# Performance work log

Measured on AMD Instinct MI355X. Metric: run time of the kernel, lower is better.

## Reference

```python
import jax, jax.numpy as jnp
import numpy as np

B, S, D, H = 2, 2048, 1024, 16
DK = D // H
NEG = -1.0e9

def setup_inputs() -> dict:
    key = jax.random.key(0)
    ks = jax.random.split(key, 12)
    sc = 1.0 / np.sqrt(D)
    q = jax.random.normal(ks[0], (B, S, D), jnp.float32)
    k = jax.random.normal(ks[1], (B, S, D), jnp.float32)
    v = jax.random.normal(ks[2], (B, S, D), jnp.float32)
    # causal mask: True = masked (matches masked_fill(mask == True, -1e9))
    mask = jnp.broadcast_to(jnp.triu(jnp.ones((S, S), bool), k=1)[None, None], (B, 1, S, S))
    Wq = jax.random.normal(ks[3], (D, D), jnp.float32) * sc
    bq = jnp.zeros((D,), jnp.float32)
    Wk = jax.random.normal(ks[4], (D, D), jnp.float32) * sc
    bk = jnp.zeros((D,), jnp.float32)
    Wv = jax.random.normal(ks[5], (D, D), jnp.float32) * sc
    bv = jnp.zeros((D,), jnp.float32)
    Wo = jax.random.normal(ks[6], (D, D), jnp.float32) * sc
    bo = jnp.zeros((D,), jnp.float32)
    return {"q": q, "k": k, "v": v, "mask": mask,
            "Wq": Wq, "bq": bq, "Wk": Wk, "bk": bk,
            "Wv": Wv, "bv": bv, "Wo": Wo, "bo": bo}

def reference(q, k, v, mask, Wq, bq, Wk, bk, Wv, bv, Wo, bo):
    def split_heads(x):  # [B,S,D] -> [B,H,S,DK]
        return x.reshape(B, S, H, DK).transpose(0, 2, 1, 3)
    qh = split_heads(q @ Wq + bq)
    kh = split_heads(k @ Wk + bk)
    vh = split_heads(v @ Wv + bv)
    scores = jnp.einsum('bhqd,bhkd->bhqk', qh, kh) / np.sqrt(DK)
    scores = jnp.where(mask, NEG, scores)
    p = jax.nn.softmax(scores, axis=-1)
    out = jnp.einsum('bhqk,bhkd->bhqd', p, vh)  # [B,H,S,DK]
    out = out.transpose(0, 2, 1, 3).reshape(B, S, D)
    return out @ Wo + bo
```

## Files before the change

kernel.cpp:

```cpp
#include <hip/hip_runtime.h>

#define BB 2
#define SS 2048
#define DD 1024
#define HH 16
#define DKK 64

typedef __attribute__((ext_vector_type(8))) short short8;
typedef __attribute__((ext_vector_type(4))) float floatx4;

__device__ inline float bf2f(ushort u) {
    union { unsigned int i; float f; } x; x.i = ((unsigned int)u) << 16; return x.f;
}
__device__ inline ushort f2bf(float f) {
    union { float f; unsigned int i; } x; x.f = f;
    unsigned int r = x.i + 0x7fff + ((x.i >> 16) & 1);
    return (ushort)(r >> 16);
}
__device__ inline void async_cp16(const ushort* g, ushort* l) {
    __builtin_amdgcn_global_load_lds(
        (const __attribute__((address_space(1))) unsigned int*)g,
        (__attribute__((address_space(3))) unsigned int*)l, 16, 0, 0);
}
__device__ inline unsigned int cvt_pk_bf16(float lo, float hi) {
    unsigned int r;
    asm("v_cvt_pk_bf16_f32 %0, %1, %2" : "=v"(r) : "v"(lo), "v"(hi));
    return r;
}
__device__ inline void swap32(unsigned int& a, unsigned int& b) {
    asm("v_permlane32_swap_b32 %0, %1" : "+v"(a), "+v"(b));
}
__device__ inline void swap16(unsigned int& a, unsigned int& b) {
    asm("v_permlane16_swap_b32 %0, %1" : "+v"(a), "+v"(b));
}

__global__ __launch_bounds__(256) void cvt_w4(const float* __restrict__ w0,
                                              const float* __restrict__ w1,
                                              const float* __restrict__ w2,
                                              const float* __restrict__ w3,
                                              ushort* __restrict__ o0,
                                              ushort* __restrict__ o1,
                                              ushort* __restrict__ o2,
                                              ushort* __restrict__ o3) {
    __shared__ ushort t[32][33];
    int z = blockIdx.z;
    const float* in = (z == 0) ? w0 : (z == 1) ? w1 : (z == 2) ? w2 : w3;
    ushort* out = (z == 0) ? o0 : (z == 1) ? o1 : (z == 2) ? o2 : o3;
    int bx = blockIdx.x, by = blockIdx.y, tx = threadIdx.x;
    for (int i = threadIdx.y; i < 32; i += 8)
        t[i][tx] = f2bf(in[(size_t)(by * 32 + i) * DD + bx * 32 + tx]);
    __syncthreads();
    for (int i = threadIdx.y; i < 32; i += 8)
        out[(size_t)(bx * 32 + i) * DD + by * 32 + tx] = t[tx][i];
}

__global__ __launch_bounds__(256) void cvt_qkv(const float* __restrict__ q,
                                               const float* __restrict__ k,
                                               const float* __restrict__ v,
                                               ushort* __restrict__ oq,
                                               ushort* __restrict__ ok,
                                               ushort* __restrict__ ov) {
    int z = blockIdx.z;
    const float* in = (z == 0) ? q : (z == 1) ? k : v;
    ushort* out = (z == 0) ? oq : (z == 1) ? ok : ov;
    int i = blockIdx.x * 256 + threadIdx.x;
    float4 f0 = ((const float4*)in)[i * 2];
    float4 f1 = ((const float4*)in)[i * 2 + 1];
    short8 p;
    p[0] = (short)f2bf(f0.x); p[1] = (short)f2bf(f0.y);
    p[2] = (short)f2bf(f0.z); p[3] = (short)f2bf(f0.w);
    p[4] = (short)f2bf(f1.x); p[5] = (short)f2bf(f1.y);
    p[6] = (short)f2bf(f1.z); p[7] = (short)f2bf(f1.w);
    ((short8*)out)[i] = p;
}

__global__ __launch_bounds__(256) void gemm_qkv(const ushort* __restrict__ Xq,
                                                const ushort* __restrict__ Xk,
                                                const ushort* __restrict__ Xv,
                                                const ushort* __restrict__ WtQ,
                                                const ushort* __restrict__ WtK,
                                                const ushort* __restrict__ WtV,
                                                const float* __restrict__ bq,
                                                const float* __restrict__ bk,
                                                const float* __restrict__ bv,
                                                ushort* __restrict__ qh,
                                                ushort* __restrict__ kh,
                                                ushort* __restrict__ vt) {
    constexpr int K = 1024;
    constexpr int NT = 32;
    constexpr int LDT = 136;
    __shared__ ushort smem[128 * LDT];

    int lin = blockIdx.x + ((blockIdx.y + (blockIdx.z << 5)) << 3);
    int wid = (lin & 7) * 96 + (lin >> 3);
    int z = wid >> 8;
    int rem = wid & 255;
    int by = rem >> 3, bx = rem & 7;

    const ushort* A  = (z == 0) ? Xq : (z == 1) ? Xk : Xv;
    const ushort* Bt = (z == 0) ? WtQ : (z == 1) ? WtK : WtV;
    const float* bias = (z == 0) ? bq : (z == 1) ? bk : bv;
    ushort* outp = (z == 0) ? qh : (z == 1) ? kh : vt;

    int tid = threadIdx.x;
    int wave = tid >> 6, lane = tid & 63, quad = lane >> 4, l15 = lane & 15;
    int wm = wave >> 1, wn = wave & 1;
    int rowBase = by * 128, colBase = bx * 128;

    auto stage = [&](int k0, int d) {
        int ab = d * 8192, bb2 = 4096 + d * 8192;
#pragma unroll
        for (int j = 0; j < 2; ++j) {
            int cbase = (j * 4 + wave) * 64;
            int c = cbase + lane;
            int row = c >> 2, sub = (c & 3) * 8;
            async_cp16(&A[(size_t)(rowBase + row) * K + k0 + sub], &smem[ab + cbase * 8]);
            async_cp16(&Bt[(size_t)(colBase + row) * K + k0 + sub], &smem[bb2 + cbase * 8]);
        }
    };

    floatx4 acc[4][4] = {};
    stage(0, 0);
    __syncthreads();
    for (int t = 0; t < NT; ++t) {
        if (t + 1 < NT) stage((t + 1) * 32, (t + 1) & 1);
        int ab = (t & 1) * 8192, bb2 = 4096 + (t & 1) * 8192;
        short8 af[4], bf[4];
#pragma unroll
        for (int mi = 0; mi < 4; ++mi)
            af[mi] = *(const short8*)&smem[ab + (wm * 64 + mi * 16 + l15) * 32 + quad * 8];
#pragma unroll
        for (int ni = 0; ni < 4; ++ni)
            bf[ni] = *(const short8*)&smem[bb2 + (wn * 64 + ni * 16 + l15) * 32 + quad * 8];
#pragma unroll
        for (int mi = 0; mi < 4; ++mi)
#pragma unroll
            for (int ni = 0; ni < 4; ++ni)
                acc[mi][ni] = __builtin_amdgcn_mfma_f32_16x16x32_bf16(
                    af[mi], bf[ni], acc[mi][ni], 0, 0, 0);
        __syncthreads();
    }
    if (z == 2) {
        for (int mi = 0; mi < 4; ++mi)
            for (int ni = 0; ni < 4; ++ni) {
                int c = wn * 64 + ni * 16 + l15;
                float bv = bias[colBase + c];
                for (int i = 0; i < 4; ++i) {
                    int r = wm * 64 + mi * 16 + quad * 4 + i;
                    smem[c * LDT + r] = f2bf(acc[mi][ni][i] + bv);
                }
            }
        __syncthreads();
        int b = rowBase >> 11;
        int sBase = rowBase & 2047;
#pragma unroll
        for (int u = 0; u < 8; ++u) {
            int chunk = u * 256 + tid;
            int c = chunk >> 4;
            int r = (chunk & 15) * 8;
            int col = colBase + c, h = col >> 6, dk = col & 63;
            int4 val = *(const int4*)&smem[c * LDT + r];
            *(int4*)&outp[((size_t)((b * HH + h) * DKK + dk)) * SS + sBase + r] = val;
        }
    } else {
        for (int mi = 0; mi < 4; ++mi)
            for (int ni = 0; ni < 4; ++ni) {
                int c = wn * 64 + ni * 16 + l15;
                float bv = bias[colBase + c];
                for (int i = 0; i < 4; ++i) {
                    int r = wm * 64 + mi * 16 + quad * 4 + i;
                    smem[r * LDT + c] = f2bf(acc[mi][ni][i] + bv);
                }
            }
        __syncthreads();
        int bb = rowBase >> 11;
        int sBase = rowBase & 2047;
#pragma unroll
        for (int u = 0; u < 8; ++u) {
            int chunk = u * 256 + tid;
            int r = chunk >> 4;
            int cc = (chunk & 15) * 8;
            int col = colBase + cc, hh = col >> 6, dk = col & 63;
            int4 val = *(const int4*)&smem[r * LDT + cc];
            *(int4*)&outp[((size_t)((bb * HH + hh) * SS + sBase + r)) * DKK + dk] = val;
        }
    }
}

__global__ __launch_bounds__(256) void gemm_fin(const ushort* __restrict__ A,
                                                const ushort* __restrict__ Bt,
                                                const float* __restrict__ bias,
                                                float* __restrict__ outp) {
    constexpr int K = 1024, N = 1024, NT = 32;
    __shared__ ushort smem[12288];
    int tid = threadIdx.x;
    int wave = tid >> 6, lane = tid & 63, quad = lane >> 4, l15 = lane & 15;
    int wm = wave >> 1, wn = wave & 1;

    int lin = blockIdx.x + (blockIdx.y << 3);
    int wid = (lin & 7) * 64 + (lin >> 3);
    int bx = wid & 7, by = wid >> 3;
    int rowBase = by * 64, colBase = bx * 128;

    auto stage = [&](int k0, int d) {
        int ab = d * 6144, bb2 = 2048 + d * 6144;
#pragma unroll
        for (int j = 0; j < 3; ++j) {
            int c = j * 4 + wave;
            int cbase = (c < 4) ? c * 64 : (c - 4) * 64;
            int cc = cbase + lane;
            int row = cc >> 2, sub = (cc & 3) * 8;
            if (c < 4)
                async_cp16(&A[(size_t)(rowBase + row) * K + k0 + sub], &smem[ab + cbase * 8]);
            else
                async_cp16(&Bt[(size_t)(colBase + row) * K + k0 + sub], &smem[bb2 + cbase * 8]);
        }
    };

    floatx4 acc[2][4] = {};
    stage(0, 0);
    __syncthreads();
    for (int t = 0; t < NT; ++t) {
        if (t + 1 < NT) stage((t + 1) * 32, (t + 1) & 1);
        int ab = (t & 1) * 6144, bb2 = 2048 + (t & 1) * 6144;
        short8 af[2], bf[4];
#pragma unroll
        for (int mi = 0; mi < 2; ++mi)
            af[mi] = *(const short8*)&smem[ab + (wm * 32 + mi * 16 + l15) * 32 + quad * 8];
#pragma unroll
        for (int ni = 0; ni < 4; ++ni)
            bf[ni] = *(const short8*)&smem[bb2 + (wn * 64 + ni * 16 + l15) * 32 + quad * 8];
#pragma unroll
        for (int mi = 0; mi < 2; ++mi)
#pragma unroll
            for (int ni = 0; ni < 4; ++ni)
                acc[mi][ni] = __builtin_amdgcn_mfma_f32_16x16x32_bf16(
                    af[mi], bf[ni], acc[mi][ni], 0, 0, 0);
        __syncthreads();
    }
    for (int mi = 0; mi < 2; ++mi)
        for (int ni = 0; ni < 4; ++ni) {
            int col = colBase + wn * 64 + ni * 16 + l15;
            float bv = bias[col];
            for (int i = 0; i < 4; ++i) {
                int row = rowBase + wm * 32 + mi * 16 + quad * 4 + i;
                outp[(size_t)row * N + col] = acc[mi][ni][i] + bv;
            }
        }
}

__global__ __launch_bounds__(256, 2) void flash_attn5(const ushort* __restrict__ qh,
                                                      const ushort* __restrict__ kh,
                                                      const ushort* __restrict__ vt,
                                                      ushort* __restrict__ attn) {
    constexpr int LD = 72;
    __shared__ ushort Ksm[2][64 * LD];
    __shared__ ushort Vsm[2][64 * LD];
    int tid = threadIdx.x;
    int h = blockIdx.y, b = blockIdx.z;
    int wave = tid >> 6, lane = tid & 63, quad = lane >> 4, l15 = lane & 15;
    const size_t headQK = ((size_t)(b * HH + h)) * SS * DKK;
    const size_t headV  = ((size_t)(b * HH + h)) * DKK * SS;
    int c0 = tid, r0 = c0 >> 3, s0 = (c0 & 7) * 8;
    int c1 = tid + 256, r1 = c1 >> 3, s1 = (c1 & 7) * 8;
    const int qt0 = blockIdx.x;
    const int qt1 = 31 - qt0;

    int qrow0 = qt0 * 64 + wave * 16 + l15;
    int qrow1 = qt1 * 64 + wave * 16 + l15;
    short8 q0a = *(const short8*)&qh[headQK + (size_t)qrow0 * DKK + quad * 8];
    short8 q0b = *(const short8*)&qh[headQK + (size_t)qrow0 * DKK + 32 + quad * 8];
    short8 q1a = *(const short8*)&qh[headQK + (size_t)qrow1 * DKK + quad * 8];
    short8 q1b = *(const short8*)&qh[headQK + (size_t)qrow1 * DKK + 32 + quad * 8];

    floatx4 o0[4] = {}, o1[4] = {};
    float l0 = 0.f, l1 = 0.f;
    int qsel = wave * 16 + l15;

    *(int4*)&Ksm[0][r0 * LD + s0] = *(const int4*)&kh[headQK + (size_t)r0 * DKK + s0];
    *(int4*)&Ksm[0][r1 * LD + s1] = *(const int4*)&kh[headQK + (size_t)r1 * DKK + s1];
    *(int4*)&Vsm[0][r0 * LD + s0] = *(const int4*)&vt[headV + (size_t)r0 * SS + s0];
    *(int4*)&Vsm[0][r1 * LD + s1] = *(const int4*)&vt[headV + (size_t)r1 * SS + s1];
    __syncthreads();

    for (int kt = 0; kt <= qt1; ++kt) {
        int cur = kt & 1;
        bool pre = (kt < qt1);
        bool act0 = (kt <= qt0);
        int4 kA, kB, vA, vB;
        if (pre) {
            const ushort* kp = &kh[headQK + (size_t)((kt + 1) * 64) * DKK];
            const ushort* vp = &vt[headV + (kt + 1) * 64];
            kA = *(const int4*)&kp[(size_t)r0 * DKK + s0];
            kB = *(const int4*)&kp[(size_t)r1 * DKK + s1];
            vA = *(const int4*)&vp[(size_t)r0 * SS + s0];
            vB = *(const int4*)&vp[(size_t)r1 * SS + s1];
        }
        floatx4 sv1[4], sv0[4];
#pragma unroll
        for (int cn = 0; cn < 4; ++cn) {
            short8 kf0 = *(const short8*)&Ksm[cur][(cn * 16 + l15) * LD + quad * 8];
            short8 kf1 = *(const short8*)&Ksm[cur][(cn * 16 + l15) * LD + 32 + quad * 8];
            floatx4 z = {};
            z = __builtin_amdgcn_mfma_f32_16x16x32_bf16(kf0, q1a, z, 0, 0, 0);
            z = __builtin_amdgcn_mfma_f32_16x16x32_bf16(kf1, q1b, z, 0, 0, 0);
            sv1[cn] = z;
            if (act0) {
                floatx4 y = {};
                y = __builtin_amdgcn_mfma_f32_16x16x32_bf16(kf0, q0a, y, 0, 0, 0);
                y = __builtin_amdgcn_mfma_f32_16x16x32_bf16(kf1, q0b, y, 0, 0, 0);
                sv0[cn] = y;
            }
        }
        short8 vf[2][4];
#pragma unroll
        for (int ks = 0; ks < 2; ++ks)
#pragma unroll
            for (int n = 0; n < 4; ++n)
                vf[ks][n] = *(const short8*)&Vsm[cur][(n * 16 + l15) * LD + ks * 32 + quad * 8];

        {
            bool diag = (kt == qt1);
            unsigned int pkd[4][2];
#pragma unroll
            for (int cn = 0; cn < 4; ++cn) {
#pragma unroll
                for (int i = 0; i < 4; ++i) {
                    float p = __expf(sv1[cn][i] * 0.125f);
                    if (diag && (cn * 16 + quad * 4 + i) > qsel) p = 0.f;
                    sv1[cn][i] = p;
                    l1 += p;
                }
                pkd[cn][0] = cvt_pk_bf16(sv1[cn][0], sv1[cn][1]);
                pkd[cn][1] = cvt_pk_bf16(sv1[cn][2], sv1[cn][3]);
            }
#pragma unroll
            for (int ks = 0; ks < 2; ++ks) {
                unsigned int a0 = pkd[ks * 2][0], b0 = pkd[ks * 2 + 1][0];
                swap32(a0, b0); swap16(a0, b0);
                unsigned int a1 = pkd[ks * 2][1], b1 = pkd[ks * 2 + 1][1];
                swap32(a1, b1); swap16(a1, b1);
                union { int4 i4; short8 s8; } u;
                u.i4 = make_int4((int)a0, (int)a1, (int)b0, (int)b1);
#pragma unroll
                for (int n = 0; n < 4; ++n)
                    o1[n] = __builtin_amdgcn_mfma_f32_16x16x32_bf16(
                        vf[ks][n], u.s8, o1[n], 0, 0, 0);
            }
        }
        if (act0) {
            bool diag = (kt == qt0);
            unsigned int pkd[4][2];
#pragma unroll
            for (int cn = 0; cn < 4; ++cn) {
#pragma unroll
                for (int i = 0; i < 4; ++i) {
                    float p = __expf(sv0[cn][i] * 0.125f);
                    if (diag && (cn * 16 + quad * 4 + i) > qsel) p = 0.f;
                    sv0[cn][i] = p;
                    l0 += p;
                }
                pkd[cn][0] = cvt_pk_bf16(sv0[cn][0], sv0[cn][1]);
                pkd[cn][1] = cvt_pk_bf16(sv0[cn][2], sv0[cn][3]);
            }
#pragma unroll
            for (int ks = 0; ks < 2; ++ks) {
                unsigned int a0 = pkd[ks * 2][0], b0 = pkd[ks * 2 + 1][0];
                swap32(a0, b0); swap16(a0, b0);
                unsigned int a1 = pkd[ks * 2][1], b1 = pkd[ks * 2 + 1][1];
                swap32(a1, b1); swap16(a1, b1);
                union { int4 i4; short8 s8; } u;
                u.i4 = make_int4((int)a0, (int)a1, (int)b0, (int)b1);
#pragma unroll
                for (int n = 0; n < 4; ++n)
                    o0[n] = __builtin_amdgcn_mfma_f32_16x16x32_bf16(
                        vf[ks][n], u.s8, o0[n], 0, 0, 0);
            }
        }
        if (pre) {
            int nb = cur ^ 1;
            *(int4*)&Ksm[nb][r0 * LD + s0] = kA;
            *(int4*)&Ksm[nb][r1 * LD + s1] = kB;
            *(int4*)&Vsm[nb][r0 * LD + s0] = vA;
            *(int4*)&Vsm[nb][r1 * LD + s1] = vB;
        }
        __syncthreads();
    }
    l0 += __shfl_xor(l0, 16, 64); l0 += __shfl_xor(l0, 32, 64);
    l1 += __shfl_xor(l1, 16, 64); l1 += __shfl_xor(l1, 32, 64);
    float inv0 = 1.0f / l0, inv1 = 1.0f / l1;
    size_t rowOff0 = ((size_t)(b * SS + qt0 * 64 + wave * 16 + l15)) * DD + h * 64;
    size_t rowOff1 = ((size_t)(b * SS + qt1 * 64 + wave * 16 + l15)) * DD + h * 64;
#pragma unroll
    for (int n = 0; n < 4; ++n) {
        int dof = n * 16 + quad * 4;
        int2 v0, v1;
        v0.x = (int)cvt_pk_bf16(o0[n][0] * inv0, o0[n][1] * inv0);
        v0.y = (int)cvt_pk_bf16(o0[n][2] * inv0, o0[n][3] * inv0);
        v1.x = (int)cvt_pk_bf16(o1[n][0] * inv1, o1[n][1] * inv1);
        v1.y = (int)cvt_pk_bf16(o1[n][2] * inv1, o1[n][3] * inv1);
        *(int2*)&attn[rowOff0 + dof] = v0;
        *(int2*)&attn[rowOff1 + dof] = v1;
    }
}

extern "C" void kernel_launch(void* const* d_in, const int* in_sizes, int n_in,
                              void* d_out, int out_size, void* d_ws, size_t ws_size,
                              hipStream_t stream) {
    const float* q  = (const float*)d_in[0];
    const float* k  = (const float*)d_in[1];
    const float* v  = (const float*)d_in[2];
    const float* Wq = (const float*)d_in[4];
    const float* bq = (const float*)d_in[5];
    const float* Wk = (const float*)d_in[6];
    const float* bk = (const float*)d_in[7];
    const float* Wv = (const float*)d_in[8];
    const float* bv = (const float*)d_in[9];
    const float* Wo = (const float*)d_in[10];
    const float* bo = (const float*)d_in[11];

    ushort* ws   = (ushort*)d_ws;
    ushort* WtQ  = ws;
    ushort* WtK  = WtQ + (1u << 20);
    ushort* WtV  = WtK + (1u << 20);
    ushort* WtO  = WtV + (1u << 20);
    ushort* Xv   = WtO + (1u << 20);
    ushort* qh   = Xv + (4u << 20);
    ushort* kh   = qh + (4u << 20);
    ushort* vt   = kh + (4u << 20);
    ushort* Xq   = (ushort*)d_out;
    ushort* Xk   = Xq + (4u << 20);
    ushort* attn = Xv;

    cvt_w4<<<dim3(32, 32, 4), dim3(32, 8), 0, stream>>>(Wq, Wk, Wv, Wo,
                                                        WtQ, WtK, WtV, WtO);
    cvt_qkv<<<dim3(2048, 1, 3), 256, 0, stream>>>(q, k, v, Xq, Xk, Xv);

    gemm_qkv<<<dim3(8, 32, 3), 256, 0, stream>>>(Xq, Xk, Xv, WtQ, WtK, WtV,
                                                 bq, bk, bv, qh, kh, vt);

    flash_attn5<<<dim3(16, 16, 2), 256, 0, stream>>>(qh, kh, vt, attn);

    gemm_fin<<<dim3(8, 64), 256, 0, stream>>>(attn, WtO, bo, (float*)d_out);
}
```

Baseline: 246.0 us.

## Enlarge QKV GEMM tiles to 256x256 with swizzled LDS and manual waitcnt pipelining

Rewrites the QKV projection GEMM to use 512-thread blocks computing 256x256 output tiles with 8x4 MFMA accumulators per wave. LDS reads use an XOR swizzle, and explicit vmcnt waits with raw barriers replace __syncthreads so the next tile's async loads overlap compute. The epilogue now writes directly to global memory instead of staging through LDS. This raises data reuse per block and reduces sync overhead, but it launches only 192 blocks, which may underfill the GPU, and the direct stores are less coalesced.

```diff
diff --git a/kernel.cpp b/kernel.cpp
--- a/kernel.cpp
+++ b/kernel.cpp
@@ -74,116 +74,140 @@
     ((short8*)out)[i] = p;
 }
 
-__global__ __launch_bounds__(256) void gemm_qkv(const ushort* __restrict__ Xq,
-                                                const ushort* __restrict__ Xk,
-                                                const ushort* __restrict__ Xv,
-                                                const ushort* __restrict__ WtQ,
-                                                const ushort* __restrict__ WtK,
-                                                const ushort* __restrict__ WtV,
-                                                const float* __restrict__ bq,
-                                                const float* __restrict__ bk,
-                                                const float* __restrict__ bv,
-                                                ushort* __restrict__ qh,
-                                                ushort* __restrict__ kh,
-                                                ushort* __restrict__ vt) {
+__global__ __launch_bounds__(512, 2) void gemm_qkv(const ushort* __restrict__ Xq,
+                                                   const ushort* __restrict__ Xk,
+                                                   const ushort* __restrict__ Xv,
+                                                   const ushort* __restrict__ WtQ,
+                                                   const ushort* __restrict__ WtK,
+                                                   const ushort* __restrict__ WtV,
+                                                   const float* __restrict__ bq,
+                                                   const float* __restrict__ bk,
+                                                   const float* __restrict__ bv,
+                                                   ushort* __restrict__ qh,
+                                                   ushort* __restrict__ kh,
+                                                   ushort* __restrict__ vt) {
     constexpr int K = 1024;
-    constexpr int NT = 32;
-    constexpr int LDT = 136;
-    __shared__ ushort smem[128 * LDT];
-
-    int lin = blockIdx.x + ((blockIdx.y + (blockIdx.z << 5)) << 3);
-    int wid = (lin & 7) * 96 + (lin >> 3);
-    int z = wid >> 8;
-    int rem = wid & 255;
-    int by = rem >> 3, bx = rem & 7;
-
-    const ushort* A  = (z == 0) ? Xq : (z == 1) ? Xk : Xv;
-    const ushort* Bt = (z == 0) ? WtQ : (z == 1) ? WtK : WtV;
+    constexpr int NKT = 32;
+    __shared__ ushort smem[32768];
+
+    int lin = blockIdx.x + (blockIdx.y << 2) + (blockIdx.z << 6);
+    int wid = (lin & 7) * 24 + (lin >> 3);
+    int z = wid >> 6;
+    int rem = wid & 63;
+    int byy = rem >> 2, bxx = rem & 3;
+    int rowBase = byy * 256, colBase = bxx * 256;
+
+    const ushort* Ag = (z == 0) ? Xq : (z == 1) ? Xk : Xv;
+    const ushort* Bg = (z == 0) ? WtQ : (z == 1) ? WtK : WtV;
     const float* bias = (z == 0) ? bq : (z == 1) ? bk : bv;
     ushort* outp = (z == 0) ? qh : (z == 1) ? kh : vt;
 
     int tid = threadIdx.x;
     int wave = tid >> 6, lane = tid & 63, quad = lane >> 4, l15 = lane & 15;
-    int wm = wave >> 1, wn = wave & 1;
-    int rowBase = by * 128, colBase = bx * 128;
-
-    auto stage = [&](int k0, int d) {
-        int ab = d * 8192, bb2 = 4096 + d * 8192;
-#pragma unroll
-        for (int j = 0; j < 2; ++j) {
-            int cbase = (j * 4 + wave) * 64;
-            int c = cbase + lane;
-            int row = c >> 2, sub = (c & 3) * 8;
-            async_cp16(&A[(size_t)(rowBase + row) * K + k0 + sub], &smem[ab + cbase * 8]);
-            async_cp16(&Bt[(size_t)(colBase + row) * K + k0 + sub], &smem[bb2 + cbase * 8]);
-        }
+    int wm = wave >> 2, wn = wave & 3;
+
+    size_t srcA[2], srcB[2];
+    int dstU[2];
+#pragma unroll
+    for (int r = 0; r < 2; ++r) {
+        int lb = r * 8192 + wave * 1024 + lane * 16;
+        int sl = lb ^ (((lb >> 9) & 1) << 5);
+        int srow = sl >> 6;
+        int scol = (sl & 63) >> 1;
+        srcA[r] = (size_t)(rowBase + srow) * K + scol;
+        srcB[r] = (size_t)(colBase + srow) * K + scol;
+        dstU[r] = r * 4096 + wave * 512;
+    }
+    int aOff[2][4], bOff[4];
+#pragma unroll
+    for (int mh = 0; mh < 2; ++mh)
+#pragma unroll
+        for (int mi = 0; mi < 4; ++mi) {
+            int row = wm * 128 + mh * 64 + mi * 16 + l15;
+            aOff[mh][mi] = row * 32 + ((quad * 8) ^ (((row >> 3) & 1) << 4));
+        }
+#pragma unroll
+    for (int ni = 0; ni < 4; ++ni) {
+        int row = wn * 64 + ni * 16 + l15;
+        bOff[ni] = 8192 + row * 32 + ((quad * 8) ^ (((row >> 3) & 1) << 4));
+    }
+
+    auto stageTile = [&](int u) {
+        int slot = (u & 1) << 14;
+        const ushort* As = Ag + u * 32;
+        const ushort* Bs = Bg + u * 32;
+        async_cp16(As + srcA[0], &smem[slot + dstU[0]]);
+        async_cp16(As + srcA[1], &smem[slot + dstU[1]]);
+        async_cp16(Bs + srcB[0], &smem[slot + 8192 + dstU[0]]);
+        async_cp16(Bs + srcB[1], &smem[slot + 8192 + dstU[1]]);
     };
 
-    floatx4 acc[4][4] = {};
-    stage(0, 0);
-    __syncthreads();
-    for (int t = 0; t < NT; ++t) {
-        if (t + 1 < NT) stage((t + 1) * 32, (t + 1) & 1);
-        int ab = (t & 1) * 8192, bb2 = 4096 + (t & 1) * 8192;
-        short8 af[4], bf[4];
-#pragma unroll
-        for (int mi = 0; mi < 4; ++mi)
-            af[mi] = *(const short8*)&smem[ab + (wm * 64 + mi * 16 + l15) * 32 + quad * 8];
+    floatx4 acc[8][4] = {};
+    stageTile(0);
+    for (int t = 0; t < NKT; ++t) {
+        if (t < NKT - 1) {
+            stageTile(t + 1);
+            asm volatile("s_waitcnt vmcnt(4)" ::: "memory");
+        } else {
+            asm volatile("s_waitcnt vmcnt(0)" ::: "memory");
+        }
+        __builtin_amdgcn_s_barrier();
+        __builtin_amdgcn_sched_barrier(0);
+        int slot = (t & 1) << 14;
+        short8 bfr[4];
 #pragma unroll
         for (int ni = 0; ni < 4; ++ni)
-            bf[ni] = *(const short8*)&smem[bb2 + (wn * 64 + ni * 16 + l15) * 32 + quad * 8];
-#pragma unroll
-        for (int mi = 0; mi < 4; ++mi)
-#pragma unroll
-            for (int ni = 0; ni < 4; ++ni)
-                acc[mi][ni] = __builtin_amdgcn_mfma_f32_16x16x32_bf16(
-                    af[mi], bf[ni], acc[mi][ni], 0, 0, 0);
-        __syncthreads();
-    }
+            bfr[ni] = *(const short8*)&smem[slot + bOff[ni]];
+#pragma unroll
+        for (int mh = 0; mh < 2; ++mh) {
+            short8 af[4];
+#pragma unroll
+            for (int mi = 0; mi < 4; ++mi)
+                af[mi] = *(const short8*)&smem[slot + aOff[mh][mi]];
+#pragma unroll
+            for (int mi = 0; mi < 4; ++mi)
+#pragma unroll
+                for (int ni = 0; ni < 4; ++ni)
+                    acc[mh * 4 + mi][ni] = __builtin_amdgcn_mfma_f32_16x16x32_bf16(
+                        af[mi], bfr[ni], acc[mh * 4 + mi][ni], 0, 0, 0);
+        }
+        __builtin_amdgcn_sched_barrier(0);
+        __builtin_amdgcn_s_barrier();
+    }
+
+    float bvv[4];
+#pragma unroll
+    for (int ni = 0; ni < 4; ++ni)
+        bvv[ni] = bias[colBase + wn * 64 + ni * 16 + l15];
     if (z == 2) {
-        for (int mi = 0; mi < 4; ++mi)
+#pragma unroll
+        for (int mi = 0; mi < 8; ++mi)
+#pragma unroll
             for (int ni = 0; ni < 4; ++ni) {
-                int c = wn * 64 + ni * 16 + l15;
-                float bv = bias[colBase + c];
+                int col = colBase + wn * 64 + ni * 16 + l15;
+                int h = col >> 6, dk = col & 63;
+                int rowg = rowBase + wm * 128 + mi * 16 + quad * 4;
+                int b = rowg >> 11, s = rowg & 2047;
+                int2 v;
+                v.x = (int)cvt_pk_bf16(acc[mi][ni][0] + bvv[ni], acc[mi][ni][1] + bvv[ni]);
+                v.y = (int)cvt_pk_bf16(acc[mi][ni][2] + bvv[ni], acc[mi][ni][3] + bvv[ni]);
+                *(int2*)&outp[((size_t)((b * HH + h) * DKK + dk)) * SS + s] = v;
+            }
+    } else {
+#pragma unroll
+        for (int mi = 0; mi < 8; ++mi)
+#pragma unroll
+            for (int ni = 0; ni < 4; ++ni) {
+                int col = colBase + wn * 64 + ni * 16 + l15;
+                int h = col >> 6, dk = col & 63;
+#pragma unroll
                 for (int i = 0; i < 4; ++i) {
-                    int r = wm * 64 + mi * 16 + quad * 4 + i;
-                    smem[c * LDT + r] = f2bf(acc[mi][ni][i] + bv);
+                    int rowg = rowBase + wm * 128 + mi * 16 + quad * 4 + i;
+                    int b = rowg >> 11, s = rowg & 2047;
+                    outp[((size_t)((b * HH + h) * SS + s)) * DKK + dk] =
+                        f2bf(acc[mi][ni][i] + bvv[ni]);
                 }
             }
-        __syncthreads();
-        int b = rowBase >> 11;
-        int sBase = rowBase & 2047;
-#pragma unroll
-        for (int u = 0; u < 8; ++u) {
-            int chunk = u * 256 + tid;
-            int c = chunk >> 4;
-            int r = (chunk & 15) * 8;
-            int col = colBase + c, h = col >> 6, dk = col & 63;
-            int4 val = *(const int4*)&smem[c * LDT + r];
-            *(int4*)&outp[((size_t)((b * HH + h) * DKK + dk)) * SS + sBase + r] = val;
-        }
-    } else {
-        for (int mi = 0; mi < 4; ++mi)
-            for (int ni = 0; ni < 4; ++ni) {
-                int c = wn * 64 + ni * 16 + l15;
-                float bv = bias[colBase + c];
-                for (int i = 0; i < 4; ++i) {
-                    int r = wm * 64 + mi * 16 + quad * 4 + i;
-                    smem[r * LDT + c] = f2bf(acc[mi][ni][i] + bv);
-                }
-            }
-        __syncthreads();
-        int bb = rowBase >> 11;
-        int sBase = rowBase & 2047;
-#pragma unroll
-        for (int u = 0; u < 8; ++u) {
-            int chunk = u * 256 + tid;
-            int r = chunk >> 4;
-            int cc = (chunk & 15) * 8;
-            int col = colBase + cc, hh = col >> 6, dk = col & 63;
-            int4 val = *(const int4*)&smem[r * LDT + cc];
-            *(int4*)&outp[((size_t)((bb * HH + hh) * SS + sBase + r)) * DKK + dk] = val;
-        }
     }
 }
 
@@ -301,10 +325,10 @@
         for (int cn = 0; cn < 4; ++cn) {
             short8 kf0 = *(const short8*)&Ksm[cur][(cn * 16 + l15) * LD + quad * 8];
             short8 kf1 = *(const short8*)&Ksm[cur][(cn * 16 + l15) * LD + 32 + quad * 8];
-            floatx4 z = {};
-            z = __builtin_amdgcn_mfma_f32_16x16x32_bf16(kf0, q1a, z, 0, 0, 0);
-            z = __builtin_amdgcn_mfma_f32_16x16x32_bf16(kf1, q1b, z, 0, 0, 0);
-            sv1[cn] = z;
+            floatx4 zz = {};
+            zz = __builtin_amdgcn_mfma_f32_16x16x32_bf16(kf0, q1a, zz, 0, 0, 0);
+            zz = __builtin_amdgcn_mfma_f32_16x16x32_bf16(kf1, q1b, zz, 0, 0, 0);
+            sv1[cn] = zz;
             if (act0) {
                 floatx4 y = {};
                 y = __builtin_amdgcn_mfma_f32_16x16x32_bf16(kf0, q0a, y, 0, 0, 0);
@@ -436,7 +460,7 @@
                                                         WtQ, WtK, WtV, WtO);
     cvt_qkv<<<dim3(2048, 1, 3), 256, 0, stream>>>(q, k, v, Xq, Xk, Xv);
 
-    gemm_qkv<<<dim3(8, 32, 3), 256, 0, stream>>>(Xq, Xk, Xv, WtQ, WtK, WtV,
+    gemm_qkv<<<dim3(4, 16, 3), 512, 0, stream>>>(Xq, Xk, Xv, WtQ, WtK, WtV,
                                                  bq, bk, bv, qh, kh, vt);
 
     flash_attn5<<<dim3(16, 16, 2), 256, 0, stream>>>(qh, kh, vt, attn);
```

Result: no change. 241.6 us (-1.8%).
